# Kernel optimization log

Measured on AMD Instinct MI355X. Metric: run time of the kernel, lower is better.

Reference implementation:

```python
import jax, jax.numpy as jnp
import numpy as np

EPS_F = 1e-6  # epsilon used when normalizing F^T F (as in EIGNN/MGNNI)


def _g(F):
    # g(F) = F^T F / (||F^T F||_F + eps): symmetric PSD, spectral radius <= 1
    FF = F.T @ F
    return FF / (jnp.linalg.norm(FF) + EPS_F)


def setup_inputs() -> dict:
    m, n = 128, 8192
    key = jax.random.key(0)
    k1, k2, k3, k4 = jax.random.split(key, 4)
    X = jax.random.normal(k1, (m, n), dtype=jnp.float32)
    # learned mixing matrix, init 1/sqrt(m) * randn as in __init__
    F = (1.0 / np.sqrt(m)) * jax.random.normal(k2, (m, m), dtype=jnp.float32)
    # precomputed eigendecomposition of the (normalized) adjacency S:
    # eigenvector matrix Q_S (n,n) and eigenvalues Lambda_S stored as (n,1)
    Q_S = jax.random.normal(k3, (n, n), dtype=jnp.float32) / np.sqrt(n)
    Lambda_S = (0.99 * (2.0 * jax.random.uniform(k4, (n, 1), dtype=jnp.float32) - 1.0))
    gamma = jnp.float32(0.8)
    return {"X": X, "F": F, "Q_S": Q_S, "Lambda_S": Lambda_S, "gamma": gamma}


def reference(X, F, Q_S, Lambda_S, gamma):
    # IDMFunction.forward: closed-form solve of Z = gamma * g(F) Z S + X
    # via eigendecompositions g(F) = Q_F diag(Lam_F) Q_F^T, S = Q_S diag(Lam_S) Q_S^T
    Lam_F, Q_F = jnp.linalg.eigh(_g(F))                         # (m,), (m,m)
    # G[i,j] = 1 / (1 - gamma * Lam_F[i] * Lam_S[j])            # (m,n)
    G = 1.0 / (1.0 - gamma * Lam_F[:, None] * Lambda_S.reshape(1, -1))
    # Z = Q_F (G * (Q_F^T X Q_S)) Q_S^T                          # (m,n)
    Z = Q_F @ (G * (Q_F.T @ X @ Q_S)) @ Q_S.T
    return Z
```

## Files before the change

kernel.cpp:

```cpp
#include <hip/hip_runtime.h>
#include <math.h>

#define EPS_F 1e-6f

typedef __attribute__((ext_vector_type(8))) short short8;
typedef __attribute__((ext_vector_type(4))) float f32x4;
typedef unsigned long long ull;

static __device__ __forceinline__ unsigned short f2bf(float f) {
    unsigned u = __float_as_uint(f);
    u += 0x7fff + ((u >> 16) & 1);
    return (unsigned short)(u >> 16);
}
static __device__ __forceinline__ ull pack4(float a, float b, float c, float d) {
    return (ull)f2bf(a) | ((ull)f2bf(b) << 16) | ((ull)f2bf(c) << 32) | ((ull)f2bf(d) << 48);
}


__global__ void kff(const float* __restrict__ F, float* __restrict__ FF) {
    int i = blockIdx.x, j = threadIdx.x;
    float s = 0.f;
    for (int k = 0; k < 128; ++k) s += F[k*128 + i] * F[k*128 + j];
    FF[i*128 + j] = s;
}

__global__ void knorm(const float* __restrict__ FF, float* __restrict__ inv) {
    float s = 0.f;
    for (int idx = threadIdx.x; idx < 128*128; idx += 256) { float v = FF[idx]; s += v*v; }
    for (int o = 32; o > 0; o >>= 1) s += __shfl_down(s, o);
    __shared__ float wsum[4];
    int lane = threadIdx.x & 63, w = threadIdx.x >> 6;
    if (lane == 0) wsum[w] = s;
    __syncthreads();
    if (threadIdx.x == 0) inv[0] = 1.f / (sqrtf(wsum[0]+wsum[1]+wsum[2]+wsum[3]) + EPS_F);
}

__global__ void kdvec(const float* __restrict__ lam, const float* __restrict__ gam,
                      float* __restrict__ D, int n) {
    int i = blockIdx.x*blockDim.x + threadIdx.x;
    if (i < n) D[i] = gam[0]*lam[i];
}

template<bool TRANSB>
__global__ __launch_bounds__(256) void gemm_mfma(
    const float* __restrict__ A, const float* __restrict__ B,
    float* __restrict__ C, int N, int K, int kChunk)
{
    constexpr int LDT = 40;
    __shared__ short As[128 * LDT];
    __shared__ short Bs[128 * LDT];

    const int t    = threadIdx.x;
    const int lane = t & 63;
    const int w    = t >> 6;
    const int wm   = (w >> 1) * 64;
    const int wn   = (w & 1)  * 64;
    const int l16  = lane & 15;
    const int lq   = lane >> 4;
    const int n0   = blockIdx.x * 128;
    const int k_beg = blockIdx.y * kChunk;

    f32x4 acc[4][4];
    #pragma unroll
    for (int i = 0; i < 4; ++i)
        #pragma unroll
        for (int j = 0; j < 4; ++j) acc[i][j] = (f32x4){0.f,0.f,0.f,0.f};

    const int bn = t & 127, bkh = t >> 7;

    for (int k0 = k_beg; k0 < k_beg + kChunk; k0 += 32) {
        #pragma unroll
        for (int i = 0; i < 4; ++i) {
            int flat = t + i*256;
            int m = flat >> 3, k4 = flat & 7;
            float4 v = *(const float4*)&A[(size_t)m*K + k0 + k4*4];
            *(ull*)&As[m*LDT + k4*4] = pack4(v.x, v.y, v.z, v.w);
        }
        if (TRANSB) {
            #pragma unroll
            for (int i = 0; i < 4; ++i) {
                int flat = t + i*256;
                int n = flat >> 3, k4 = flat & 7;
                float4 v = *(const float4*)&B[(size_t)(n0+n)*K + k0 + k4*4];
                *(ull*)&Bs[n*LDT + k4*4] = pack4(v.x, v.y, v.z, v.w);
            }
        } else {
            float vv[16];
            #pragma unroll
            for (int j = 0; j < 16; ++j)
                vv[j] = B[(size_t)(k0 + bkh*16 + j)*N + n0 + bn];
            short8 p0, p1;
            #pragma unroll
            for (int j = 0; j < 8; ++j) { p0[j] = (short)f2bf(vv[j]); p1[j] = (short)f2bf(vv[j+8]); }
            *(short8*)&Bs[bn*LDT + bkh*16    ] = p0;
            *(short8*)&Bs[bn*LDT + bkh*16 + 8] = p1;
        }
        __syncthreads();

        short8 a[4], b[4];
        #pragma unroll
        for (int mt = 0; mt < 4; ++mt)
            a[mt] = *(const short8*)&As[(wm + mt*16 + l16)*LDT + lq*8];
        #pragma unroll
        for (int nt = 0; nt < 4; ++nt)
            b[nt] = *(const short8*)&Bs[(wn + nt*16 + l16)*LDT + lq*8];
        #pragma unroll
        for (int mt = 0; mt < 4; ++mt)
            #pragma unroll
            for (int nt = 0; nt < 4; ++nt)
                acc[mt][nt] = __builtin_amdgcn_mfma_f32_16x16x32_bf16(a[mt], b[nt], acc[mt][nt], 0, 0, 0);
        __syncthreads();
    }

    #pragma unroll
    for (int mt = 0; mt < 4; ++mt)
        #pragma unroll
        for (int nt = 0; nt < 4; ++nt)
            #pragma unroll
            for (int r = 0; r < 4; ++r) {
                int row = wm + mt*16 + lq*4 + r;
                int col = n0 + wn + nt*16 + l16;
                atomicAdd(&C[(size_t)row*N + col], acc[mt][nt][r]);
            }
}

__global__ __launch_bounds__(512) void horner_fused(
    const float* __restrict__ FF, const float* __restrict__ invn,
    const float* __restrict__ D, const float* __restrict__ Y,
    float* __restrict__ R, int N)
{
    constexpr int LDT = 136;
    constexpr int T = 14;
    __shared__ short Abf[128 * LDT];
    __shared__ short Rbf[32 * LDT];

    const int t    = threadIdx.x;
    const int lane = t & 63;
    const int w    = t >> 6;
    const int wm   = (w >> 1) * 32;
    const int wn   = (w & 1) * 16;
    const int l16  = lane & 15;
    const int lq   = lane >> 4;
    const int j0   = blockIdx.x * 32;

    #pragma unroll
    for (int i = 0; i < 8; ++i) {
        int flat = t + i*512;
        int m = flat >> 5, k4 = flat & 31;
        float4 v = *(const float4*)&FF[m*128 + k4*4];
        *(ull*)&Abf[m*LDT + k4*4] = pack4(v.x, v.y, v.z, v.w);
    }
    {
        int j = t & 31, mg = t >> 5;
        float vv[8];
        #pragma unroll
        for (int r2 = 0; r2 < 8; ++r2)
            vv[r2] = Y[(size_t)(mg*8 + r2)*N + j0 + j];
        *(ull*)&Rbf[j*LDT + mg*8    ] = pack4(vv[0], vv[1], vv[2], vv[3]);
        *(ull*)&Rbf[j*LDT + mg*8 + 4] = pack4(vv[4], vv[5], vv[6], vv[7]);
    }
    const int col = j0 + wn + l16;
    float yreg[2][4];
    #pragma unroll
    for (int mt = 0; mt < 2; ++mt)
        #pragma unroll
        for (int r = 0; r < 4; ++r)
            yreg[mt][r] = Y[(size_t)(wm + mt*16 + lq*4 + r)*N + col];
    const float s = D[col] * invn[0];

    for (int it = 0; it < T; ++it) {
        __syncthreads();
        f32x4 racc[2];
        racc[0] = (f32x4){0.f,0.f,0.f,0.f};
        racc[1] = (f32x4){0.f,0.f,0.f,0.f};
        #pragma unroll
        for (int kq = 0; kq < 4; ++kq) {
            short8 b  = *(const short8*)&Rbf[(wn + l16)*LDT + kq*32 + lq*8];
            short8 a0 = *(const short8*)&Abf[(wm      + l16)*LDT + kq*32 + lq*8];
            short8 a1 = *(const short8*)&Abf[(wm + 16 + l16)*LDT + kq*32 + lq*8];
            racc[0] = __builtin_amdgcn_mfma_f32_16x16x32_bf16(a0, b, racc[0], 0, 0, 0);
            racc[1] = __builtin_amdgcn_mfma_f32_16x16x32_bf16(a1, b, racc[1], 0, 0, 0);
        }
        __syncthreads();
        #pragma unroll
        for (int mt = 0; mt < 2; ++mt) {
            float r0 = yreg[mt][0] + s*racc[mt][0];
            float r1 = yreg[mt][1] + s*racc[mt][1];
            float r2 = yreg[mt][2] + s*racc[mt][2];
            float r3 = yreg[mt][3] + s*racc[mt][3];
            if (it < T-1) {
                *(ull*)&Rbf[(wn + l16)*LDT + wm + mt*16 + lq*4] = pack4(r0, r1, r2, r3);
            } else {
                int row = wm + mt*16 + lq*4;
                R[(size_t)(row+0)*N + col] = r0;
                R[(size_t)(row+1)*N + col] = r1;
                R[(size_t)(row+2)*N + col] = r2;
                R[(size_t)(row+3)*N + col] = r3;
            }
        }
    }
}


extern "C" void kernel_launch(void* const* d_in, const int* in_sizes, int n_in,
                              void* d_out, int out_size, void* d_ws, size_t ws_size,
                              hipStream_t stream) {
    const float* X   = (const float*)d_in[0];
    const float* F   = (const float*)d_in[1];
    const float* Q   = (const float*)d_in[2];
    const float* lam = (const float*)d_in[3];
    const float* gam = (const float*)d_in[4];
    float* Z = (float*)d_out;

    const int M = 128, N = 8192, K = 8192;

    char* ws = (char*)d_ws;
    float* FF  = (float*)(ws);
    float* inv = (float*)(ws + 65536);
    float* D   = (float*)(ws + 65792);
    float* Y   = (float*)(ws + 131072);
    float* RA  = (float*)(ws + 131072 + 4194304);

    hipLaunchKernelGGL(kff,   dim3(128), dim3(128), 0, stream, F, FF);
    hipLaunchKernelGGL(knorm, dim3(1),   dim3(256), 0, stream, FF, inv);
    hipLaunchKernelGGL(kdvec, dim3(32),  dim3(256), 0, stream, lam, gam, D, N);

    hipMemsetAsync(Y, 0, (size_t)M*N*sizeof(float), stream);
    hipLaunchKernelGGL((gemm_mfma<false>), dim3(64, 8), dim3(256), 0, stream,
                       X, Q, Y, N, K, 1024);

    hipLaunchKernelGGL(horner_fused, dim3(256), dim3(512), 0, stream,
                       FF, inv, D, Y, RA, N);

    hipMemsetAsync(Z, 0, (size_t)M*N*sizeof(float), stream);
    hipLaunchKernelGGL((gemm_mfma<true>), dim3(64, 8), dim3(256), 0, stream,
                       RA, Q, Z, N, K, 1024);
}
```

Measured before the change: 186.0 us.

## Pre-convert X to bf16, split-K partial buffers, and direct-register GEMM2

X is converted to bf16 once in a separate kernel, and both GEMMs stop restaging the 128-row operand through shared memory: they load bf16 fragments directly from global memory. GEMM1 writes per-K-split partial results into separate buffers that the Horner kernel sums, replacing the memset and atomics. Horner now emits its result in bf16, and GEMM2 reads Q rows straight into MFMA operands without shared memory. The goal is less HBM traffic, fewer atomics and fewer shared-memory copies. The costs are 32 MB of extra partial-buffer traffic and repeated uncached-pattern global loads of the small operand.

New measurement: 303.7 us. +63.3%, slower.

```diff
diff --git a/kernel.cpp b/kernel.cpp
--- a/kernel.cpp
+++ b/kernel.cpp
@@ -14,6 +14,9 @@
 }
 static __device__ __forceinline__ ull pack4(float a, float b, float c, float d) {
     return (ull)f2bf(a) | ((ull)f2bf(b) << 16) | ((ull)f2bf(c) << 32) | ((ull)f2bf(d) << 48);
+}
+static __device__ __forceinline__ float bf2f(unsigned short s) {
+    return __uint_as_float(((unsigned)s) << 16);
 }
 
 
@@ -35,104 +38,85 @@
     if (threadIdx.x == 0) inv[0] = 1.f / (sqrtf(wsum[0]+wsum[1]+wsum[2]+wsum[3]) + EPS_F);
 }
 
-__global__ void kdvec(const float* __restrict__ lam, const float* __restrict__ gam,
-                      float* __restrict__ D, int n) {
+__global__ void kxbf(const float* __restrict__ X, short* __restrict__ Xb) {
     int i = blockIdx.x*blockDim.x + threadIdx.x;
-    if (i < n) D[i] = gam[0]*lam[i];
-}
-
-template<bool TRANSB>
-__global__ __launch_bounds__(256) void gemm_mfma(
-    const float* __restrict__ A, const float* __restrict__ B,
-    float* __restrict__ C, int N, int K, int kChunk)
+    const float4* p = (const float4*)(X + (size_t)i*8);
+    float4 v0 = p[0], v1 = p[1];
+    *(ull*)&Xb[(size_t)i*8    ] = pack4(v0.x, v0.y, v0.z, v0.w);
+    *(ull*)&Xb[(size_t)i*8 + 4] = pack4(v1.x, v1.y, v1.z, v1.w);
+}
+
+__global__ __launch_bounds__(256, 4) void gemm1(
+    const short* __restrict__ Xb, const float* __restrict__ Q,
+    float* __restrict__ Yp, int N, int K)
 {
     constexpr int LDT = 40;
-    __shared__ short As[128 * LDT];
-    __shared__ short Bs[128 * LDT];
+    constexpr int KC  = 1024;
+    __shared__ short Bs[64 * LDT];
 
     const int t    = threadIdx.x;
     const int lane = t & 63;
     const int w    = t >> 6;
     const int wm   = (w >> 1) * 64;
-    const int wn   = (w & 1)  * 64;
+    const int wn   = (w & 1)  * 32;
     const int l16  = lane & 15;
     const int lq   = lane >> 4;
-    const int n0   = blockIdx.x * 128;
-    const int k_beg = blockIdx.y * kChunk;
-
-    f32x4 acc[4][4];
-    #pragma unroll
-    for (int i = 0; i < 4; ++i)
-        #pragma unroll
-        for (int j = 0; j < 4; ++j) acc[i][j] = (f32x4){0.f,0.f,0.f,0.f};
-
-    const int bn = t & 127, bkh = t >> 7;
-
-    for (int k0 = k_beg; k0 < k_beg + kChunk; k0 += 32) {
-        #pragma unroll
-        for (int i = 0; i < 4; ++i) {
-            int flat = t + i*256;
-            int m = flat >> 3, k4 = flat & 7;
-            float4 v = *(const float4*)&A[(size_t)m*K + k0 + k4*4];
-            *(ull*)&As[m*LDT + k4*4] = pack4(v.x, v.y, v.z, v.w);
-        }
-        if (TRANSB) {
+    const int n0   = blockIdx.x * 64;
+    const int kb   = blockIdx.y * KC;
+    const int bn   = t & 63, bkh = t >> 6;
+
+    float* Yout = Yp + (size_t)blockIdx.y * (128 * 8192);
+
+    f32x4 acc[4][2];
+    #pragma unroll
+    for (int i = 0; i < 4; ++i) { acc[i][0] = (f32x4){0,0,0,0}; acc[i][1] = (f32x4){0,0,0,0}; }
+
+    for (int k0 = kb; k0 < kb + KC; k0 += 32) {
+        short8 a[4];
+        #pragma unroll
+        for (int mt = 0; mt < 4; ++mt)
+            a[mt] = *(const short8*)&Xb[(size_t)(wm + mt*16 + l16)*K + k0 + lq*8];
+
+        float vv[8];
+        #pragma unroll
+        for (int j = 0; j < 8; ++j)
+            vv[j] = Q[(size_t)(k0 + bkh*8 + j)*N + n0 + bn];
+        short8 p;
+        #pragma unroll
+        for (int j = 0; j < 8; ++j) p[j] = (short)f2bf(vv[j]);
+        *(short8*)&Bs[bn*LDT + bkh*8] = p;
+        __syncthreads();
+
+        short8 b[2];
+        b[0] = *(const short8*)&Bs[(wn      + l16)*LDT + lq*8];
+        b[1] = *(const short8*)&Bs[(wn + 16 + l16)*LDT + lq*8];
+        #pragma unroll
+        for (int mt = 0; mt < 4; ++mt) {
+            acc[mt][0] = __builtin_amdgcn_mfma_f32_16x16x32_bf16(a[mt], b[0], acc[mt][0], 0, 0, 0);
+            acc[mt][1] = __builtin_amdgcn_mfma_f32_16x16x32_bf16(a[mt], b[1], acc[mt][1], 0, 0, 0);
+        }
+        __syncthreads();
+    }
+
+    #pragma unroll
+    for (int mt = 0; mt < 4; ++mt)
+        #pragma unroll
+        for (int nt = 0; nt < 2; ++nt)
             #pragma unroll
-            for (int i = 0; i < 4; ++i) {
-                int flat = t + i*256;
-                int n = flat >> 3, k4 = flat & 7;
-                float4 v = *(const float4*)&B[(size_t)(n0+n)*K + k0 + k4*4];
-                *(ull*)&Bs[n*LDT + k4*4] = pack4(v.x, v.y, v.z, v.w);
-            }
-        } else {
-            float vv[16];
-            #pragma unroll
-            for (int j = 0; j < 16; ++j)
-                vv[j] = B[(size_t)(k0 + bkh*16 + j)*N + n0 + bn];
-            short8 p0, p1;
-            #pragma unroll
-            for (int j = 0; j < 8; ++j) { p0[j] = (short)f2bf(vv[j]); p1[j] = (short)f2bf(vv[j+8]); }
-            *(short8*)&Bs[bn*LDT + bkh*16    ] = p0;
-            *(short8*)&Bs[bn*LDT + bkh*16 + 8] = p1;
-        }
-        __syncthreads();
-
-        short8 a[4], b[4];
-        #pragma unroll
-        for (int mt = 0; mt < 4; ++mt)
-            a[mt] = *(const short8*)&As[(wm + mt*16 + l16)*LDT + lq*8];
-        #pragma unroll
-        for (int nt = 0; nt < 4; ++nt)
-            b[nt] = *(const short8*)&Bs[(wn + nt*16 + l16)*LDT + lq*8];
-        #pragma unroll
-        for (int mt = 0; mt < 4; ++mt)
-            #pragma unroll
-            for (int nt = 0; nt < 4; ++nt)
-                acc[mt][nt] = __builtin_amdgcn_mfma_f32_16x16x32_bf16(a[mt], b[nt], acc[mt][nt], 0, 0, 0);
-        __syncthreads();
-    }
-
-    #pragma unroll
-    for (int mt = 0; mt < 4; ++mt)
-        #pragma unroll
-        for (int nt = 0; nt < 4; ++nt)
-            #pragma unroll
-            for (int r = 0; r < 4; ++r) {
-                int row = wm + mt*16 + lq*4 + r;
-                int col = n0 + wn + nt*16 + l16;
-                atomicAdd(&C[(size_t)row*N + col], acc[mt][nt][r]);
-            }
+            for (int r = 0; r < 4; ++r)
+                Yout[(size_t)(wm + mt*16 + lq*4 + r)*N + n0 + wn + nt*16 + l16] = acc[mt][nt][r];
 }
 
 __global__ __launch_bounds__(512) void horner_fused(
     const float* __restrict__ FF, const float* __restrict__ invn,
-    const float* __restrict__ D, const float* __restrict__ Y,
-    float* __restrict__ R, int N)
+    const float* __restrict__ lam, const float* __restrict__ gam,
+    const float* __restrict__ Yp, short* __restrict__ Rg, int N)
 {
     constexpr int LDT = 136;
     constexpr int T = 14;
+    constexpr int SPL = 8;
     __shared__ short Abf[128 * LDT];
-    __shared__ short Rbf[32 * LDT];
+    __shared__ short Rs[32 * LDT];
 
     const int t    = threadIdx.x;
     const int lane = t & 63;
@@ -154,28 +138,34 @@
         int j = t & 31, mg = t >> 5;
         float vv[8];
         #pragma unroll
-        for (int r2 = 0; r2 < 8; ++r2)
-            vv[r2] = Y[(size_t)(mg*8 + r2)*N + j0 + j];
-        *(ull*)&Rbf[j*LDT + mg*8    ] = pack4(vv[0], vv[1], vv[2], vv[3]);
-        *(ull*)&Rbf[j*LDT + mg*8 + 4] = pack4(vv[4], vv[5], vv[6], vv[7]);
-    }
+        for (int r2 = 0; r2 < 8; ++r2) {
+            size_t idx = (size_t)(mg*8 + r2)*N + j0 + j;
+            float s = 0.f;
+            #pragma unroll
+            for (int sp = 0; sp < SPL; ++sp) s += Yp[(size_t)sp*(128*8192) + idx];
+            vv[r2] = s;
+        }
+        *(ull*)&Rs[j*LDT + mg*8    ] = pack4(vv[0], vv[1], vv[2], vv[3]);
+        *(ull*)&Rs[j*LDT + mg*8 + 4] = pack4(vv[4], vv[5], vv[6], vv[7]);
+    }
+    __syncthreads();
+
     const int col = j0 + wn + l16;
     float yreg[2][4];
     #pragma unroll
     for (int mt = 0; mt < 2; ++mt)
         #pragma unroll
         for (int r = 0; r < 4; ++r)
-            yreg[mt][r] = Y[(size_t)(wm + mt*16 + lq*4 + r)*N + col];
-    const float s = D[col] * invn[0];
+            yreg[mt][r] = bf2f((unsigned short)Rs[(wn + l16)*LDT + wm + mt*16 + lq*4 + r]);
+    const float s = gam[0] * lam[col] * invn[0];
 
     for (int it = 0; it < T; ++it) {
-        __syncthreads();
         f32x4 racc[2];
-        racc[0] = (f32x4){0.f,0.f,0.f,0.f};
-        racc[1] = (f32x4){0.f,0.f,0.f,0.f};
+        racc[0] = (f32x4){0,0,0,0};
+        racc[1] = (f32x4){0,0,0,0};
         #pragma unroll
         for (int kq = 0; kq < 4; ++kq) {
-            short8 b  = *(const short8*)&Rbf[(wn + l16)*LDT + kq*32 + lq*8];
+            short8 b  = *(const short8*)&Rs[(wn + l16)*LDT + kq*32 + lq*8];
             short8 a0 = *(const short8*)&Abf[(wm      + l16)*LDT + kq*32 + lq*8];
             short8 a1 = *(const short8*)&Abf[(wm + 16 + l16)*LDT + kq*32 + lq*8];
             racc[0] = __builtin_amdgcn_mfma_f32_16x16x32_bf16(a0, b, racc[0], 0, 0, 0);
@@ -189,16 +179,61 @@
             float r2 = yreg[mt][2] + s*racc[mt][2];
             float r3 = yreg[mt][3] + s*racc[mt][3];
             if (it < T-1) {
-                *(ull*)&Rbf[(wn + l16)*LDT + wm + mt*16 + lq*4] = pack4(r0, r1, r2, r3);
+                *(ull*)&Rs[(wn + l16)*LDT + wm + mt*16 + lq*4] = pack4(r0, r1, r2, r3);
             } else {
                 int row = wm + mt*16 + lq*4;
-                R[(size_t)(row+0)*N + col] = r0;
-                R[(size_t)(row+1)*N + col] = r1;
-                R[(size_t)(row+2)*N + col] = r2;
-                R[(size_t)(row+3)*N + col] = r3;
+                Rg[(size_t)(row+0)*N + col] = (short)f2bf(r0);
+                Rg[(size_t)(row+1)*N + col] = (short)f2bf(r1);
+                Rg[(size_t)(row+2)*N + col] = (short)f2bf(r2);
+                Rg[(size_t)(row+3)*N + col] = (short)f2bf(r3);
             }
         }
-    }
+        if (it < T-1) __syncthreads();
+    }
+}
+
+__global__ __launch_bounds__(256, 3) void gemm2(
+    const short* __restrict__ Rb, const float* __restrict__ Q,
+    float* __restrict__ Z, int N, int K)
+{
+    constexpr int KC = 1024;
+    const int t    = threadIdx.x;
+    const int lane = t & 63;
+    const int w    = t >> 6;
+    const int l16  = lane & 15;
+    const int lq   = lane >> 4;
+    const int i0   = blockIdx.x * 64 + w * 16;
+    const int kb   = blockIdx.y * KC;
+
+    f32x4 acc[8];
+    #pragma unroll
+    for (int i = 0; i < 8; ++i) acc[i] = (f32x4){0,0,0,0};
+
+    const size_t qrow = (size_t)(i0 + l16) * K;
+
+    #pragma unroll 2
+    for (int k0 = kb; k0 < kb + KC; k0 += 32) {
+        float4 q0 = *(const float4*)&Q[qrow + k0 + lq*8];
+        float4 q1 = *(const float4*)&Q[qrow + k0 + lq*8 + 4];
+        short8 a[8];
+        #pragma unroll
+        for (int mt = 0; mt < 8; ++mt)
+            a[mt] = *(const short8*)&Rb[(size_t)(mt*16 + l16)*K + k0 + lq*8];
+        short8 b;
+        b[0] = (short)f2bf(q0.x); b[1] = (short)f2bf(q0.y);
+        b[2] = (short)f2bf(q0.z); b[3] = (short)f2bf(q0.w);
+        b[4] = (short)f2bf(q1.x); b[5] = (short)f2bf(q1.y);
+        b[6] = (short)f2bf(q1.z); b[7] = (short)f2bf(q1.w);
+        #pragma unroll
+        for (int mt = 0; mt < 8; ++mt)
+            acc[mt] = __builtin_amdgcn_mfma_f32_16x16x32_bf16(a[mt], b, acc[mt], 0, 0, 0);
+    }
+
+    #pragma unroll
+    for (int mt = 0; mt < 8; ++mt)
+        #pragma unroll
+        for (int r = 0; r < 4; ++r)
+            atomicAdd(&Z[(size_t)(mt*16 + lq*4 + r)*N + i0 + l16], acc[mt][r]);
 }
 
 
@@ -212,27 +247,24 @@
     const float* gam = (const float*)d_in[4];
     float* Z = (float*)d_out;
 
-    const int M = 128, N = 8192, K = 8192;
+    const int N = 8192, K = 8192;
 
     char* ws = (char*)d_ws;
     float* FF  = (float*)(ws);
     float* inv = (float*)(ws + 65536);
-    float* D   = (float*)(ws + 65792);
-    float* Y   = (float*)(ws + 131072);
-    float* RA  = (float*)(ws + 131072 + 4194304);
+    short* Xb  = (short*)(ws + 131072);
+    short* Rg  = (short*)(ws + 131072 + 2097152);
+    float* Yp  = (float*)(ws + 131072 + 4194304);
 
     hipLaunchKernelGGL(kff,   dim3(128), dim3(128), 0, stream, F, FF);
     hipLaunchKernelGGL(knorm, dim3(1),   dim3(256), 0, stream, FF, inv);
-    hipLaunchKernelGGL(kdvec, dim3(32),  dim3(256), 0, stream, lam, gam, D, N);
-
-    hipMemsetAsync(Y, 0, (size_t)M*N*sizeof(float), stream);
-    hipLaunchKernelGGL((gemm_mfma<false>), dim3(64, 8), dim3(256), 0, stream,
-                       X, Q, Y, N, K, 1024);
+    hipLaunchKernelGGL(kxbf,  dim3(512), dim3(256), 0, stream, X, Xb);
+
+    hipLaunchKernelGGL(gemm1, dim3(128, 8), dim3(256), 0, stream, Xb, Q, Yp, N, K);
 
     hipLaunchKernelGGL(horner_fused, dim3(256), dim3(512), 0, stream,
-                       FF, inv, D, Y, RA, N);
-
-    hipMemsetAsync(Z, 0, (size_t)M*N*sizeof(float), stream);
-    hipLaunchKernelGGL((gemm_mfma<true>), dim3(64, 8), dim3(256), 0, stream,
-                       RA, Q, Z, N, K, 1024);
-}
+                       FF, inv, lam, gam, Yp, Rg, N);
+
+    hipMemsetAsync(Z, 0, (size_t)128*N*sizeof(float), stream);
+    hipLaunchKernelGGL(gemm2, dim3(128, 8), dim3(256), 0, stream, Rg, Q, Z, N, K);
+}
```
